# Kernel tuning notes

Measured on AMD Instinct MI355X. Metric: run time of the kernel, lower is better.

## Reference

```python
import jax, jax.numpy as jnp
import numpy as np

B, S, D = 8, 2048, 1024


def setup_inputs() -> dict:
    key = jax.random.key(0)
    ks = jax.random.split(key, 7)
    scale = 1.0 / np.sqrt(D)
    return {
        "tensor_sequence": jax.random.normal(ks[0], (B, S, D), dtype=jnp.float32),
        "Wq": jax.random.normal(ks[1], (D, D), dtype=jnp.float32) * scale,
        "bq": jax.random.normal(ks[2], (D,), dtype=jnp.float32) * scale,
        "Wk": jax.random.normal(ks[3], (D, D), dtype=jnp.float32) * scale,
        "bk": jax.random.normal(ks[4], (D,), dtype=jnp.float32) * scale,
        "Wv": jax.random.normal(ks[5], (D, D), dtype=jnp.float32) * scale,
        "bv": jax.random.normal(ks[6], (D,), dtype=jnp.float32) * scale,
    }


def reference(tensor_sequence, Wq, bq, Wk, bk, Wv, bv):
    # torch.nn.Linear: y = x @ W.T + b
    q = jnp.einsum("bsd,ed->bse", tensor_sequence, Wq) + bq
    k = jnp.einsum("bsd,ed->bse", tensor_sequence, Wk) + bk
    v = jnp.einsum("bsd,ed->bse", tensor_sequence, Wv) + bv
    scores = jnp.einsum("bqd,bkd->bqk", q, k)            # [B,S,S]
    weights = jax.nn.softmax(scores, axis=-1)
    attention = weights.sum(axis=-1)                      # [B,S] (== ones mathematically)
    out = jnp.einsum("bsf,bs->bf", v, attention)          # [B,D]
    return out
```

## Files before the change

kernel.cpp:

```cpp
#include <hip/hip_runtime.h>

#define BB 8
#define SS 2048
#define DD 1024


__global__ __launch_bounds__(256) void colsum_direct(
    const float* __restrict__ x, float* __restrict__ xs) {
    const int bid = blockIdx.x;
    const int b  = bid >> 5;
    const int dt = bid & 31;
    const int t  = threadIdx.x;
    const int f4 = t & 7;
    const int rg = t >> 3;
    const int lane = t & 63;
    const int w  = t >> 6;

    const float* xb = x + (size_t)b * SS * DD + dt * 32;
    float4 a = make_float4(0.f, 0.f, 0.f, 0.f);
#pragma unroll 16
    for (int it = 0; it < SS / 32; ++it) {
        const int r = it * 32 + rg;
        float4 v = ((const float4*)(xb + (size_t)r * DD))[f4];
        a.x += v.x; a.y += v.y; a.z += v.z; a.w += v.w;
    }
#pragma unroll
    for (int off = 8; off <= 32; off <<= 1) {
        a.x += __shfl_xor(a.x, off);
        a.y += __shfl_xor(a.y, off);
        a.z += __shfl_xor(a.z, off);
        a.w += __shfl_xor(a.w, off);
    }
    __shared__ float4 lds[4][8];
    if (lane < 8) lds[w][lane] = a;
    __syncthreads();
    if (t < 8) {
        float4 s0 = lds[0][t], s1 = lds[1][t], s2 = lds[2][t], s3 = lds[3][t];
        float4 r4;
        r4.x = s0.x + s1.x + s2.x + s3.x;
        r4.y = s0.y + s1.y + s2.y + s3.y;
        r4.z = s0.z + s1.z + s2.z + s3.z;
        r4.w = s0.w + s1.w + s2.w + s3.w;
        ((float4*)xs)[bid * 8 + t] = r4;
    }
}

__global__ __launch_bounds__(256) void gemv_out(
    const float* __restrict__ Wv, const float* __restrict__ bv,
    const float* __restrict__ xs, float* __restrict__ out) {
    const int e = blockIdx.x;
    const int t = threadIdx.x;
    const int lane = t & 63;
    const int wid = t >> 6;

    const float4 w = ((const float4*)(Wv + (size_t)e * DD))[t];

    float acc[BB];
#pragma unroll
    for (int b = 0; b < BB; ++b) {
        float4 xv = ((const float4*)(xs + b * DD))[t];
        acc[b] = w.x * xv.x + w.y * xv.y + w.z * xv.z + w.w * xv.w;
    }

    __shared__ float lds[BB * 4];
#pragma unroll
    for (int b = 0; b < BB; ++b) {
        float v = acc[b];
#pragma unroll
        for (int off = 32; off > 0; off >>= 1) v += __shfl_down(v, off);
        if (lane == 0) lds[b * 4 + wid] = v;
    }
    __syncthreads();
    if (t < BB) {
        out[(size_t)t * DD + e] = lds[t * 4 + 0] + lds[t * 4 + 1]
                                + lds[t * 4 + 2] + lds[t * 4 + 3]
                                + (float)SS * bv[e];
    }
}

extern "C" void kernel_launch(void* const* d_in, const int* in_sizes, int n_in,
                              void* d_out, int out_size, void* d_ws, size_t ws_size,
                              hipStream_t stream) {
    const float* x  = (const float*)d_in[0];
    const float* Wv = (const float*)d_in[5];
    const float* bv = (const float*)d_in[6];
    float* out = (float*)d_out;

    float* xs = (float*)d_ws;

    colsum_direct<<<BB * 32, 256, 0, stream>>>(x, xs);
    gemv_out<<<DD, 256, 0, stream>>>(Wv, bv, xs, out);
}
```

Baseline: 21.26 us.

## Split column-sum over sequence chunks with partial buffers and a separate reduce kernel

```diff
diff --git a/kernel.cpp b/kernel.cpp
--- a/kernel.cpp
+++ b/kernel.cpp
@@ -3,26 +3,33 @@
 #define BB 8
 #define SS 2048
 #define DD 1024
+#define SC 8
+#define NI4 (BB * DD / 4)
+
+using f4 = __attribute__((ext_vector_type(4))) float;
 
 
-__global__ __launch_bounds__(256) void colsum_direct(
-    const float* __restrict__ x, float* __restrict__ xs) {
+__global__ __launch_bounds__(256) void colsum_part(
+    const float* __restrict__ x, float* __restrict__ part) {
     const int bid = blockIdx.x;
-    const int b  = bid >> 5;
-    const int dt = bid & 31;
-    const int t  = threadIdx.x;
-    const int f4 = t & 7;
-    const int rg = t >> 3;
+    const int b    = bid >> 8;
+    const int rest = bid & 255;
+    const int dt   = rest >> 3;
+    const int sc   = rest & 7;
+    const int t    = threadIdx.x;
+    const int f4i  = t & 7;
+    const int rg   = t >> 3;
     const int lane = t & 63;
-    const int w  = t >> 6;
+    const int w    = t >> 6;
 
-    const float* xb = x + (size_t)b * SS * DD + dt * 32;
-    float4 a = make_float4(0.f, 0.f, 0.f, 0.f);
-#pragma unroll 16
-    for (int it = 0; it < SS / 32; ++it) {
+    const f4* xp = (const f4*)(x + (size_t)b * SS * DD
+                                 + (size_t)sc * (SS / SC) * DD + dt * 32);
+    f4 a = (f4)(0.f);
+#pragma unroll
+    for (int it = 0; it < (SS / SC) / 32; ++it) {
         const int r = it * 32 + rg;
-        float4 v = ((const float4*)(xb + (size_t)r * DD))[f4];
-        a.x += v.x; a.y += v.y; a.z += v.z; a.w += v.w;
+        f4 v = __builtin_nontemporal_load(&xp[(size_t)r * (DD / 4) + f4i]);
+        a += v;
     }
 #pragma unroll
     for (int off = 8; off <= 32; off <<= 1) {
@@ -31,18 +38,23 @@
         a.z += __shfl_xor(a.z, off);
         a.w += __shfl_xor(a.w, off);
     }
-    __shared__ float4 lds[4][8];
+    __shared__ f4 lds[4][8];
     if (lane < 8) lds[w][lane] = a;
     __syncthreads();
     if (t < 8) {
-        float4 s0 = lds[0][t], s1 = lds[1][t], s2 = lds[2][t], s3 = lds[3][t];
-        float4 r4;
-        r4.x = s0.x + s1.x + s2.x + s3.x;
-        r4.y = s0.y + s1.y + s2.y + s3.y;
-        r4.z = s0.z + s1.z + s2.z + s3.z;
-        r4.w = s0.w + s1.w + s2.w + s3.w;
-        ((float4*)xs)[bid * 8 + t] = r4;
+        f4 r4 = lds[0][t] + lds[1][t] + lds[2][t] + lds[3][t];
+        ((f4*)part)[(size_t)sc * NI4 + b * 256 + dt * 8 + t] = r4;
     }
+}
+
+__global__ __launch_bounds__(256) void colsum_reduce(
+    const float* __restrict__ part, float* __restrict__ xs) {
+    const int i4 = blockIdx.x * 256 + threadIdx.x;
+    const f4* p = (const f4*)part;
+    f4 a = (f4)(0.f);
+#pragma unroll
+    for (int sc = 0; sc < SC; ++sc) a += p[(size_t)sc * NI4 + i4];
+    ((f4*)xs)[i4] = a;
 }
 
 __global__ __launch_bounds__(256) void gemv_out(
@@ -53,12 +65,12 @@
     const int lane = t & 63;
     const int wid = t >> 6;
 
-    const float4 w = ((const float4*)(Wv + (size_t)e * DD))[t];
+    const f4 w = ((const f4*)(Wv + (size_t)e * DD))[t];
 
     float acc[BB];
 #pragma unroll
     for (int b = 0; b < BB; ++b) {
-        float4 xv = ((const float4*)(xs + b * DD))[t];
+        f4 xv = ((const f4*)(xs + b * DD))[t];
         acc[b] = w.x * xv.x + w.y * xv.y + w.z * xv.z + w.w * xv.w;
     }
 
@@ -86,8 +98,10 @@
     const float* bv = (const float*)d_in[6];
     float* out = (float*)d_out;
 
-    float* xs = (float*)d_ws;
+    float* part = (float*)d_ws;
+    float* xs   = part + (size_t)SC * BB * DD;
 
-    colsum_direct<<<BB * 32, 256, 0, stream>>>(x, xs);
+    colsum_part<<<2048, 256, 0, stream>>>(x, part);
+    colsum_reduce<<<SC, 256, 0, stream>>>(part, xs);
     gemv_out<<<DD, 256, 0, stream>>>(Wv, bv, xs, out);
 }
```

Measured after the change: 23.26 us. +9.4%, slower.

## Fuse column-sum with partial Wv matvec and add small split-K reduction kernel

Applied to the files above, without the earlier changes.

```diff
diff --git a/kernel.cpp b/kernel.cpp
--- a/kernel.cpp
+++ b/kernel.cpp
@@ -4,25 +4,28 @@
 #define SS 2048
 #define DD 1024
 
+using f4 = __attribute__((ext_vector_type(4))) float;
 
-__global__ __launch_bounds__(256) void colsum_direct(
-    const float* __restrict__ x, float* __restrict__ xs) {
+
+__global__ __launch_bounds__(256) void colsum_matvec(
+    const float* __restrict__ x, const float* __restrict__ Wv,
+    float* __restrict__ contrib)
+{
     const int bid = blockIdx.x;
-    const int b  = bid >> 5;
-    const int dt = bid & 31;
-    const int t  = threadIdx.x;
-    const int f4 = t & 7;
-    const int rg = t >> 3;
+    const int b   = bid >> 5;
+    const int dt  = bid & 31;
+    const int t   = threadIdx.x;
+    const int f4i = t & 7;
+    const int rg  = t >> 3;
     const int lane = t & 63;
-    const int w  = t >> 6;
+    const int w    = t >> 6;
 
     const float* xb = x + (size_t)b * SS * DD + dt * 32;
-    float4 a = make_float4(0.f, 0.f, 0.f, 0.f);
+    f4 a = (f4)(0.f);
 #pragma unroll 16
     for (int it = 0; it < SS / 32; ++it) {
         const int r = it * 32 + rg;
-        float4 v = ((const float4*)(xb + (size_t)r * DD))[f4];
-        a.x += v.x; a.y += v.y; a.z += v.z; a.w += v.w;
+        a += ((const f4*)(xb + (size_t)r * DD))[f4i];
     }
 #pragma unroll
     for (int off = 8; off <= 32; off <<= 1) {
@@ -31,51 +34,40 @@
         a.z += __shfl_xor(a.z, off);
         a.w += __shfl_xor(a.w, off);
     }
-    __shared__ float4 lds[4][8];
+    __shared__ f4 lds[4][8];
+    __shared__ f4 sl4[8];
     if (lane < 8) lds[w][lane] = a;
     __syncthreads();
-    if (t < 8) {
-        float4 s0 = lds[0][t], s1 = lds[1][t], s2 = lds[2][t], s3 = lds[3][t];
-        float4 r4;
-        r4.x = s0.x + s1.x + s2.x + s3.x;
-        r4.y = s0.y + s1.y + s2.y + s3.y;
-        r4.z = s0.z + s1.z + s2.z + s3.z;
-        r4.w = s0.w + s1.w + s2.w + s3.w;
-        ((float4*)xs)[bid * 8 + t] = r4;
+    if (t < 8) sl4[t] = lds[0][t] + lds[1][t] + lds[2][t] + lds[3][t];
+    __syncthreads();
+
+    const int er = lane >> 3;
+    const int k4 = lane & 7;
+    const f4 slv = sl4[k4];
+#pragma unroll 4
+    for (int p = 0; p < 32; ++p) {
+        const int e = w * 256 + p * 8 + er;
+        const f4 wv = ((const f4*)(Wv + (size_t)e * DD + dt * 32))[k4];
+        float d = wv.x * slv.x + wv.y * slv.y + wv.z * slv.z + wv.w * slv.w;
+        d += __shfl_xor(d, 1);
+        d += __shfl_xor(d, 2);
+        d += __shfl_xor(d, 4);
+        if (k4 == 0) contrib[(size_t)bid * DD + e] = d;
     }
 }
 
-__global__ __launch_bounds__(256) void gemv_out(
-    const float* __restrict__ Wv, const float* __restrict__ bv,
-    const float* __restrict__ xs, float* __restrict__ out) {
-    const int e = blockIdx.x;
-    const int t = threadIdx.x;
-    const int lane = t & 63;
-    const int wid = t >> 6;
-
-    const float4 w = ((const float4*)(Wv + (size_t)e * DD))[t];
-
-    float acc[BB];
+__global__ __launch_bounds__(256) void contrib_reduce(
+    const float* __restrict__ contrib, const float* __restrict__ bv,
+    float* __restrict__ out)
+{
+    const int i = blockIdx.x * 256 + threadIdx.x;
+    const int b = i >> 10;
+    const int e = i & 1023;
+    float s = 0.f;
 #pragma unroll
-    for (int b = 0; b < BB; ++b) {
-        float4 xv = ((const float4*)(xs + b * DD))[t];
-        acc[b] = w.x * xv.x + w.y * xv.y + w.z * xv.z + w.w * xv.w;
-    }
-
-    __shared__ float lds[BB * 4];
-#pragma unroll
-    for (int b = 0; b < BB; ++b) {
-        float v = acc[b];
-#pragma unroll
-        for (int off = 32; off > 0; off >>= 1) v += __shfl_down(v, off);
-        if (lane == 0) lds[b * 4 + wid] = v;
-    }
-    __syncthreads();
-    if (t < BB) {
-        out[(size_t)t * DD + e] = lds[t * 4 + 0] + lds[t * 4 + 1]
-                                + lds[t * 4 + 2] + lds[t * 4 + 3]
-                                + (float)SS * bv[e];
-    }
+    for (int dt = 0; dt < 32; ++dt)
+        s += contrib[((size_t)(b * 32 + dt)) * DD + e];
+    out[i] = s + (float)SS * bv[e];
 }
 
 extern "C" void kernel_launch(void* const* d_in, const int* in_sizes, int n_in,
@@ -86,8 +78,8 @@
     const float* bv = (const float*)d_in[6];
     float* out = (float*)d_out;
 
-    float* xs = (float*)d_ws;
+    float* contrib = (float*)d_ws;
 
-    colsum_direct<<<BB * 32, 256, 0, stream>>>(x, xs);
-    gemv_out<<<DD, 256, 0, stream>>>(Wv, bv, xs, out);
+    colsum_matvec<<<BB * 32, 256, 0, stream>>>(x, Wv, contrib);
+    contrib_reduce<<<32, 256, 0, stream>>>(contrib, bv, out);
 }
```

After: 30.72 us. 44.5% more time.
